# Kernel tuning notes

Measured on AMD Instinct MI355X. Metric: run time of the kernel, lower is better.

## Reference

```python
import jax, jax.numpy as jnp
import numpy as np

N_NODES = 100000
N_EDGES = 3200000
N_FEAT = 512
HIDDEN = 16
N_LABELS = 64


def gcn_layer(x, frm, to, W, b, n_nodes):
    # Original removes existing self-loops then adds one self-loop per node.
    # Equivalent jit-friendly form: zero-mask self-loop edges, add +1 to every
    # node's degree and an explicit self-loop term deg^-0.5 * deg^-0.5 * xw.
    mask = (frm != to).astype(x.dtype)                      # [E]
    deg = jax.ops.segment_sum(mask, to, num_segments=n_nodes) + 1.0  # [N], >=1 so no inf
    dis = deg ** -0.5                                        # [N]
    ew = dis[frm] * mask * dis[to]                           # [E]
    xw = x @ W                                               # [N, out]
    msgs = xw[frm] * ew[:, None]                             # gather-multiply  [E, out]
    agg = jax.ops.segment_sum(msgs, to, num_segments=n_nodes)  # scatter-add [N, out]
    out = agg + xw * (dis * dis)[:, None] + b                # self-loop weight = dis[i]^2
    return out


def setup_inputs() -> dict:
    key = jax.random.key(0)
    k1, k2, k3, k4 = jax.random.split(key, 4)
    x = jax.random.normal(k1, (N_NODES, N_FEAT), dtype=jnp.float32)
    edge_index = jax.random.randint(k2, (2, N_EDGES), 0, N_NODES, dtype=jnp.int32)
    # Xavier-uniform linear weights, zero bias (reset_paramters)
    lim1 = float(np.sqrt(6.0 / (N_FEAT + HIDDEN)))
    W1 = jax.random.uniform(k3, (N_FEAT, HIDDEN), jnp.float32, -lim1, lim1)
    b1 = jnp.zeros((HIDDEN,), jnp.float32)
    lim2 = float(np.sqrt(6.0 / (HIDDEN + N_LABELS)))
    W2 = jax.random.uniform(k4, (HIDDEN, N_LABELS), jnp.float32, -lim2, lim2)
    b2 = jnp.zeros((N_LABELS,), jnp.float32)
    return {"x": x, "edge_index": edge_index, "W1": W1, "b1": b1, "W2": W2, "b2": b2}


def reference(x, edge_index, W1, b1, W2, b2):
    n = x.shape[0]
    frm, to = edge_index[0], edge_index[1]
    h = jax.nn.relu(gcn_layer(x, frm, to, W1, b1, n))
    # dropout is identity in eval mode
    logits = gcn_layer(h, frm, to, W2, b2, n)
    return jax.nn.log_softmax(logits, axis=1)
```

## Files before the change

kernel.cpp:

```cpp
#include <hip/hip_runtime.h>
#include <hip/hip_fp16.h>
#include <cstdint>
#include <cstddef>

#define N_NODES 100000
#define N_FEAT  512
#define HIDDEN  16
#define N_LABELS 64
#define N_EDGES 3200000

#define NB    782
#define NPAD  (NB * 128)
#define CAP   4608
#define EPB   4096
#define BIN_BLOCKS 782
#define SPLITK 4

static const size_t O_GCUR = 0;
static const size_t O_DIS  = (size_t)16 << 10;
static const size_t O_STA  = (size_t)420 << 10;
static const size_t O_END  = (size_t)824 << 10;
static const size_t O_XWS  = (size_t)1228 << 10;
static const size_t O_HS   = (size_t)4360 << 10;
static const size_t O_TMP  = (size_t)7492 << 10;
static const size_t O_PART = (size_t)21572 << 10;
#define PART_STRIDE_H ((size_t)NPAD * 16)

__global__ __launch_bounds__(512) void k_bin(const int* __restrict__ frm,
                                             const int* __restrict__ to,
                                             int* __restrict__ gcur,
                                             unsigned* __restrict__ tmp) {
    __shared__ unsigned short barr[EPB];
    __shared__ int hist[NB + 1];
    __shared__ int gbase[NB];
    __shared__ int lcur[NB];
    const int t = threadIdx.x;
    const size_t e0 = (size_t)blockIdx.x * EPB;

    for (int i = t; i < NB + 1; i += 512) hist[i] = 0;
    __syncthreads();

    #pragma unroll
    for (int i = t; i < EPB; i += 512) {
        size_t e = e0 + i;
        int b = NB;
        if (e < N_EDGES) {
            int f = frm[e], tt = to[e];
            if (f != tt) b = tt >> 7;
        }
        barr[i] = (unsigned short)b;
        atomicAdd(&hist[b], 1);
    }
    __syncthreads();

    for (int b = t; b < NB; b += 512) {
        gbase[b] = atomicAdd(&gcur[b], hist[b]);
        lcur[b] = 0;
    }
    __syncthreads();

    #pragma unroll
    for (int i = t; i < EPB; i += 512) {
        int b = barr[i];
        if (b < NB) {
            size_t e = e0 + i;
            int f = frm[e], tt = to[e];
            int r = atomicAdd(&lcur[b], 1);
            int p = gbase[b] + r;
            if (p < CAP)
                tmp[(size_t)b * CAP + p] = ((unsigned)f << 7) | (unsigned)(tt & 127);
        }
    }
}

__global__ __launch_bounds__(512) void k_sort(unsigned* __restrict__ tmp,
                                              const int* __restrict__ gcur,
                                              int* __restrict__ starts,
                                              int* __restrict__ ends,
                                              float* __restrict__ dis) {
    __shared__ unsigned stage[CAP];
    __shared__ int cnt[128];
    __shared__ int sc[128];
    __shared__ int lcur[128];
    const int t = threadIdx.x, b = blockIdx.x;
    const int n_e = min(gcur[b], CAP);
    unsigned* seg = tmp + (size_t)b * CAP;

    if (t < 128) { cnt[t] = 0; lcur[t] = 0; }
    __syncthreads();

    for (int i = t; i < n_e; i += 512) {
        unsigned w = seg[i];
        stage[i] = w;
        atomicAdd(&cnt[w & 127u], 1);
    }
    __syncthreads();

    if (t < 128) sc[t] = cnt[t];
    __syncthreads();
    #pragma unroll
    for (int off = 1; off < 128; off <<= 1) {
        int a = 0;
        if (t < 128 && t >= off) a = sc[t - off];
        __syncthreads();
        if (t < 128) sc[t] += a;
        __syncthreads();
    }

    if (t < 128) {
        int excl = sc[t] - cnt[t];
        int node = b * 128 + t;
        int s0 = b * CAP + excl;
        starts[node] = s0;
        ends[node]   = s0 + cnt[t];
        dis[node]    = rsqrtf((float)cnt[t] + 1.0f);
    }
    __syncthreads();

    for (int i = t; i < n_e; i += 512) {
        unsigned w = stage[i];
        int tl = (int)(w & 127u);
        int p = atomicAdd(&lcur[tl], 1);
        seg[(sc[tl] - cnt[tl]) + p] = w >> 7;
    }
}

#define KT 32
__global__ __launch_bounds__(256) void k_gemm1(const float* __restrict__ x,
                                               const float* __restrict__ W1,
                                               __half* __restrict__ part) {
    __shared__ float xs[256 * 33];
    const int t = threadIdx.x;
    const int base = blockIdx.x * 256;
    const int kb = blockIdx.y * (N_FEAT / SPLITK);
    float acc[HIDDEN];
    #pragma unroll
    for (int j = 0; j < HIDDEN; ++j) acc[j] = 0.f;

    const int pr = t >> 3;
    const int pc = (t & 7) * 4;

    for (int kt = 0; kt < N_FEAT / SPLITK / KT; ++kt) {
        __syncthreads();
        #pragma unroll
        for (int p = 0; p < 8; ++p) {
            int r = p * 32 + pr;
            int n = base + r;
            float4 v = make_float4(0.f, 0.f, 0.f, 0.f);
            if (n < N_NODES)
                v = *(const float4*)(x + (size_t)n * N_FEAT + kb + kt * KT + pc);
            xs[r * 33 + pc + 0] = v.x;
            xs[r * 33 + pc + 1] = v.y;
            xs[r * 33 + pc + 2] = v.z;
            xs[r * 33 + pc + 3] = v.w;
        }
        __syncthreads();
        #pragma unroll
        for (int kk = 0; kk < KT; ++kk) {
            float xv = xs[t * 33 + kk];
            const float4* wr = (const float4*)(W1 + ((size_t)(kb + kt * KT + kk) << 4));
            float4 wa = wr[0], wb = wr[1], wc = wr[2], wd = wr[3];
            acc[ 0] = fmaf(xv, wa.x, acc[ 0]);
            acc[ 1] = fmaf(xv, wa.y, acc[ 1]);
            acc[ 2] = fmaf(xv, wa.z, acc[ 2]);
            acc[ 3] = fmaf(xv, wa.w, acc[ 3]);
            acc[ 4] = fmaf(xv, wb.x, acc[ 4]);
            acc[ 5] = fmaf(xv, wb.y, acc[ 5]);
            acc[ 6] = fmaf(xv, wb.z, acc[ 6]);
            acc[ 7] = fmaf(xv, wb.w, acc[ 7]);
            acc[ 8] = fmaf(xv, wc.x, acc[ 8]);
            acc[ 9] = fmaf(xv, wc.y, acc[ 9]);
            acc[10] = fmaf(xv, wc.z, acc[10]);
            acc[11] = fmaf(xv, wc.w, acc[11]);
            acc[12] = fmaf(xv, wd.x, acc[12]);
            acc[13] = fmaf(xv, wd.y, acc[13]);
            acc[14] = fmaf(xv, wd.z, acc[14]);
            acc[15] = fmaf(xv, wd.w, acc[15]);
        }
    }
    int n = base + t;
    if (n < N_NODES) {
        __half2 h2[8];
        #pragma unroll
        for (int j = 0; j < 8; ++j)
            h2[j] = __float22half2_rn(make_float2(acc[2 * j], acc[2 * j + 1]));
        float4* o = (float4*)(part + (size_t)blockIdx.y * PART_STRIDE_H + (size_t)n * HIDDEN);
        o[0] = *(float4*)&h2[0];
        o[1] = *(float4*)&h2[4];
    }
}

__global__ __launch_bounds__(256) void k_comb(const __half2* __restrict__ part2,
                                              const float* __restrict__ dis,
                                              __half2* __restrict__ xws2) {
    int i = blockIdx.x * 256 + threadIdx.x;
    if (i >= N_NODES * 8) return;
    const size_t st = (size_t)NPAD * 8;
    float2 a = __half22float2(part2[i]);
    float2 b = __half22float2(part2[st + i]);
    float2 c = __half22float2(part2[2 * st + i]);
    float2 d = __half22float2(part2[3 * st + i]);
    float dn = dis[i >> 3];
    xws2[i] = __float22half2_rn(make_float2(dn * (a.x + b.x + c.x + d.x),
                                            dn * (a.y + b.y + c.y + d.y)));
}

__global__ __launch_bounds__(512) void k_agg(const __half* __restrict__ rows,
                                             const unsigned* __restrict__ sorted,
                                             const int* __restrict__ starts,
                                             const int* __restrict__ ends,
                                             const float* __restrict__ dis,
                                             const float* __restrict__ bias,
                                             __half* __restrict__ outp,
                                             int mode) {
    const int t = threadIdx.x;
    const int lane = t & 15, g = t >> 4;
    const int n = blockIdx.x * 32 + g;
    const int s0 = starts[n], e0 = ends[n];
    float acc = 0.f;
    for (int base = s0; base < e0; base += 16) {
        int idx = base + lane;
        unsigned f = (idx < e0) ? sorted[idx] : 0u;
        int cnt = min(16, e0 - base);
        #pragma unroll
        for (int q = 0; q < 16; ++q) {
            unsigned fq = __shfl(f, q, 16);
            float v = __half2float(rows[(size_t)fq * HIDDEN + lane]);
            if (q < cnt) acc += v;
        }
    }
    if (n < N_NODES) {
        float dn = dis[n];
        float sum = acc + __half2float(rows[(size_t)n * HIDDEN + lane]);
        float v;
        if (mode) v = fmaxf(fmaf(dn, sum, bias[lane]), 0.f) * dn;
        else      v = dn * sum;
        outp[(size_t)n * HIDDEN + lane] = __float2half(v);
    }
}

__global__ __launch_bounds__(256) void k_out(const __half* __restrict__ z,
                                             const float* __restrict__ W2,
                                             const float* __restrict__ b2,
                                             float* __restrict__ out) {
    int gt = blockIdx.x * 256 + threadIdx.x;
    int n = gt >> 6;
    int j = gt & 63;
    float acc = b2[j];
    const __half* zr = z + (size_t)n * HIDDEN;
    #pragma unroll
    for (int k = 0; k < HIDDEN; ++k)
        acc = fmaf(__half2float(zr[k]), W2[k * N_LABELS + j], acc);
    float m = acc;
    #pragma unroll
    for (int off = 32; off > 0; off >>= 1)
        m = fmaxf(m, __shfl_xor(m, off, 64));
    float ex = __expf(acc - m);
    float sum = ex;
    #pragma unroll
    for (int off = 32; off > 0; off >>= 1)
        sum += __shfl_xor(sum, off, 64);
    out[(size_t)n * N_LABELS + j] = acc - m - __logf(sum);
}

extern "C" void kernel_launch(void* const* d_in, const int* in_sizes, int n_in,
                              void* d_out, int out_size, void* d_ws, size_t ws_size,
                              hipStream_t stream) {
    const float* x  = (const float*)d_in[0];
    const int*   ei = (const int*)d_in[1];
    const float* W1 = (const float*)d_in[2];
    const float* b1 = (const float*)d_in[3];
    const float* W2 = (const float*)d_in[4];
    const float* b2 = (const float*)d_in[5];
    float* out = (float*)d_out;
    char*  ws  = (char*)d_ws;

    int*      gcur   = (int*)(ws + O_GCUR);
    float*    dis    = (float*)(ws + O_DIS);
    int*      starts = (int*)(ws + O_STA);
    int*      ends   = (int*)(ws + O_END);
    __half*   xws    = (__half*)(ws + O_XWS);
    __half*   hs     = (__half*)(ws + O_HS);
    unsigned* tmp    = (unsigned*)(ws + O_TMP);
    __half*   part   = (__half*)(ws + O_PART);

    const int* frm = ei;
    const int* to  = ei + N_EDGES;

    hipMemsetAsync(gcur, 0, NB * sizeof(int), stream);

    k_bin  <<<BIN_BLOCKS, 512, 0, stream>>>(frm, to, gcur, tmp);
    k_sort <<<NB, 512, 0, stream>>>(tmp, gcur, starts, ends, dis);
    k_gemm1<<<dim3(391, SPLITK), 256, 0, stream>>>(x, W1, part);
    k_comb <<<3125, 256, 0, stream>>>((const __half2*)part, dis, (__half2*)xws);
    k_agg  <<<NPAD / 32, 512, 0, stream>>>(xws, tmp, starts, ends, dis, b1, hs, 1);
    k_agg  <<<NPAD / 32, 512, 0, stream>>>(hs, tmp, starts, ends, dis, b1, xws, 0);
    k_out  <<<N_NODES / 4, 256, 0, stream>>>(xws, W2, b2, out);
}
```

Baseline: 472.4 us.

## Fuse edge binning and split-K first GEMM into one heterogeneous launch

Merges the edge-binning kernel and the x@W1 split-K GEMM into a single launch. Block indices below BIN_BLOCKS do binning and the rest do GEMM tiles, so the memory-bound binning and the x streaming can overlap and one launch is saved. Binning now caches the packed edge word in shared memory so the scatter pass does not reload frm/to. The GEMM tile becomes 512 rows with a K-tile of 16 in a shared-memory union, which raises per-block shared usage and register pressure for the binning blocks and may lower occupancy.

```diff
diff --git a/kernel.cpp b/kernel.cpp
--- a/kernel.cpp
+++ b/kernel.cpp
@@ -15,6 +15,7 @@
 #define EPB   4096
 #define BIN_BLOCKS 782
 #define SPLITK 4
+#define GBLK  196
 
 static const size_t O_GCUR = 0;
 static const size_t O_DIS  = (size_t)16 << 10;
@@ -26,49 +27,131 @@
 static const size_t O_PART = (size_t)21572 << 10;
 #define PART_STRIDE_H ((size_t)NPAD * 16)
 
-__global__ __launch_bounds__(512) void k_bin(const int* __restrict__ frm,
-                                             const int* __restrict__ to,
-                                             int* __restrict__ gcur,
-                                             unsigned* __restrict__ tmp) {
-    __shared__ unsigned short barr[EPB];
-    __shared__ int hist[NB + 1];
-    __shared__ int gbase[NB];
-    __shared__ int lcur[NB];
+struct BinSh {
+    unsigned short barr[EPB];
+    unsigned       pk[EPB];
+    int hist[NB + 1];
+    int gbase[NB];
+    int lcur[NB];
+};
+union SMemBG {
+    BinSh bin;
+    float xs[512 * 17];
+};
+
+__global__ __launch_bounds__(512) void k_bg(const int* __restrict__ frm,
+                                            const int* __restrict__ to,
+                                            int* __restrict__ gcur,
+                                            unsigned* __restrict__ tmp,
+                                            const float* __restrict__ x,
+                                            const float* __restrict__ W1,
+                                            __half* __restrict__ part) {
+    __shared__ SMemBG sm;
     const int t = threadIdx.x;
-    const size_t e0 = (size_t)blockIdx.x * EPB;
-
-    for (int i = t; i < NB + 1; i += 512) hist[i] = 0;
-    __syncthreads();
-
-    #pragma unroll
-    for (int i = t; i < EPB; i += 512) {
-        size_t e = e0 + i;
-        int b = NB;
-        if (e < N_EDGES) {
-            int f = frm[e], tt = to[e];
-            if (f != tt) b = tt >> 7;
-        }
-        barr[i] = (unsigned short)b;
-        atomicAdd(&hist[b], 1);
-    }
-    __syncthreads();
-
-    for (int b = t; b < NB; b += 512) {
-        gbase[b] = atomicAdd(&gcur[b], hist[b]);
-        lcur[b] = 0;
-    }
-    __syncthreads();
-
-    #pragma unroll
-    for (int i = t; i < EPB; i += 512) {
-        int b = barr[i];
-        if (b < NB) {
+    const int bid = blockIdx.x;
+
+    if (bid < BIN_BLOCKS) {
+        BinSh& B = sm.bin;
+        const size_t e0 = (size_t)bid * EPB;
+
+        for (int i = t; i < NB + 1; i += 512) B.hist[i] = 0;
+        __syncthreads();
+
+        #pragma unroll
+        for (int i = t; i < EPB; i += 512) {
             size_t e = e0 + i;
-            int f = frm[e], tt = to[e];
-            int r = atomicAdd(&lcur[b], 1);
-            int p = gbase[b] + r;
-            if (p < CAP)
-                tmp[(size_t)b * CAP + p] = ((unsigned)f << 7) | (unsigned)(tt & 127);
+            int b = NB;
+            unsigned pk = 0;
+            if (e < N_EDGES) {
+                int f = frm[e], tt = to[e];
+                if (f != tt) {
+                    b = tt >> 7;
+                    pk = ((unsigned)f << 7) | (unsigned)(tt & 127);
+                }
+            }
+            B.barr[i] = (unsigned short)b;
+            B.pk[i] = pk;
+            atomicAdd(&B.hist[b], 1);
+        }
+        __syncthreads();
+
+        for (int b = t; b < NB; b += 512) {
+            B.gbase[b] = atomicAdd(&gcur[b], B.hist[b]);
+            B.lcur[b] = 0;
+        }
+        __syncthreads();
+
+        #pragma unroll
+        for (int i = t; i < EPB; i += 512) {
+            int b = B.barr[i];
+            if (b < NB) {
+                int r = atomicAdd(&B.lcur[b], 1);
+                int p = B.gbase[b] + r;
+                if (p < CAP)
+                    tmp[(size_t)b * CAP + p] = B.pk[i];
+            }
+        }
+    } else {
+        const int g = bid - BIN_BLOCKS;
+        const int split = g / GBLK;
+        const int bx = g - split * GBLK;
+        const int base = bx * 512;
+        const int kb = split * 128;
+
+        float acc[HIDDEN];
+        #pragma unroll
+        for (int j = 0; j < HIDDEN; ++j) acc[j] = 0.f;
+
+        const int pr = t >> 2;
+        const int pc = (t & 3) << 2;
+
+        for (int kt = 0; kt < 8; ++kt) {
+            __syncthreads();
+            #pragma unroll
+            for (int p = 0; p < 4; ++p) {
+                int r = p * 128 + pr;
+                int n = base + r;
+                float4 v = make_float4(0.f, 0.f, 0.f, 0.f);
+                if (n < N_NODES)
+                    v = *(const float4*)(x + (size_t)n * N_FEAT + kb + kt * 16 + pc);
+                sm.xs[r * 17 + pc + 0] = v.x;
+                sm.xs[r * 17 + pc + 1] = v.y;
+                sm.xs[r * 17 + pc + 2] = v.z;
+                sm.xs[r * 17 + pc + 3] = v.w;
+            }
+            __syncthreads();
+            #pragma unroll
+            for (int kk = 0; kk < 16; ++kk) {
+                float xv = sm.xs[t * 17 + kk];
+                const float4* wr = (const float4*)(W1 + ((size_t)(kb + kt * 16 + kk) << 4));
+                float4 wa = wr[0], wb = wr[1], wc = wr[2], wd = wr[3];
+                acc[ 0] = fmaf(xv, wa.x, acc[ 0]);
+                acc[ 1] = fmaf(xv, wa.y, acc[ 1]);
+                acc[ 2] = fmaf(xv, wa.z, acc[ 2]);
+                acc[ 3] = fmaf(xv, wa.w, acc[ 3]);
+                acc[ 4] = fmaf(xv, wb.x, acc[ 4]);
+                acc[ 5] = fmaf(xv, wb.y, acc[ 5]);
+                acc[ 6] = fmaf(xv, wb.z, acc[ 6]);
+                acc[ 7] = fmaf(xv, wb.w, acc[ 7]);
+                acc[ 8] = fmaf(xv, wc.x, acc[ 8]);
+                acc[ 9] = fmaf(xv, wc.y, acc[ 9]);
+                acc[10] = fmaf(xv, wc.z, acc[10]);
+                acc[11] = fmaf(xv, wc.w, acc[11]);
+                acc[12] = fmaf(xv, wd.x, acc[12]);
+                acc[13] = fmaf(xv, wd.y, acc[13]);
+                acc[14] = fmaf(xv, wd.z, acc[14]);
+                acc[15] = fmaf(xv, wd.w, acc[15]);
+            }
+        }
+        int n = base + t;
+        if (n < N_NODES) {
+            __half2 h2[8];
+            #pragma unroll
+            for (int j = 0; j < 8; ++j)
+                h2[j] = __float22half2_rn(make_float2(acc[2 * j], acc[2 * j + 1]));
+            float4* o = (float4*)(part + (size_t)split * PART_STRIDE_H + (size_t)n * HIDDEN);
+            o[0] = *(float4*)&h2[0];
+            o[1] = *(float4*)&h2[4];
         }
     }
 }
@@ -122,71 +205,6 @@
         int tl = (int)(w & 127u);
         int p = atomicAdd(&lcur[tl], 1);
         seg[(sc[tl] - cnt[tl]) + p] = w >> 7;
-    }
-}
-
-#define KT 32
-__global__ __launch_bounds__(256) void k_gemm1(const float* __restrict__ x,
-                                               const float* __restrict__ W1,
-                                               __half* __restrict__ part) {
-    __shared__ float xs[256 * 33];
-    const int t = threadIdx.x;
-    const int base = blockIdx.x * 256;
-    const int kb = blockIdx.y * (N_FEAT / SPLITK);
-    float acc[HIDDEN];
-    #pragma unroll
-    for (int j = 0; j < HIDDEN; ++j) acc[j] = 0.f;
-
-    const int pr = t >> 3;
-    const int pc = (t & 7) * 4;
-
-    for (int kt = 0; kt < N_FEAT / SPLITK / KT; ++kt) {
-        __syncthreads();
-        #pragma unroll
-        for (int p = 0; p < 8; ++p) {
-            int r = p * 32 + pr;
-            int n = base + r;
-            float4 v = make_float4(0.f, 0.f, 0.f, 0.f);
-            if (n < N_NODES)
-                v = *(const float4*)(x + (size_t)n * N_FEAT + kb + kt * KT + pc);
-            xs[r * 33 + pc + 0] = v.x;
-            xs[r * 33 + pc + 1] = v.y;
-            xs[r * 33 + pc + 2] = v.z;
-            xs[r * 33 + pc + 3] = v.w;
-        }
-        __syncthreads();
-        #pragma unroll
-        for (int kk = 0; kk < KT; ++kk) {
-            float xv = xs[t * 33 + kk];
-            const float4* wr = (const float4*)(W1 + ((size_t)(kb + kt * KT + kk) << 4));
-            float4 wa = wr[0], wb = wr[1], wc = wr[2], wd = wr[3];
-            acc[ 0] = fmaf(xv, wa.x, acc[ 0]);
-            acc[ 1] = fmaf(xv, wa.y, acc[ 1]);
-            acc[ 2] = fmaf(xv, wa.z, acc[ 2]);
-            acc[ 3] = fmaf(xv, wa.w, acc[ 3]);
-            acc[ 4] = fmaf(xv, wb.x, acc[ 4]);
-            acc[ 5] = fmaf(xv, wb.y, acc[ 5]);
-            acc[ 6] = fmaf(xv, wb.z, acc[ 6]);
-            acc[ 7] = fmaf(xv, wb.w, acc[ 7]);
-            acc[ 8] = fmaf(xv, wc.x, acc[ 8]);
-            acc[ 9] = fmaf(xv, wc.y, acc[ 9]);
-            acc[10] = fmaf(xv, wc.z, acc[10]);
-            acc[11] = fmaf(xv, wc.w, acc[11]);
-            acc[12] = fmaf(xv, wd.x, acc[12]);
-            acc[13] = fmaf(xv, wd.y, acc[13]);
-            acc[14] = fmaf(xv, wd.z, acc[14]);
-            acc[15] = fmaf(xv, wd.w, acc[15]);
-        }
-    }
-    int n = base + t;
-    if (n < N_NODES) {
-        __half2 h2[8];
-        #pragma unroll
-        for (int j = 0; j < 8; ++j)
-            h2[j] = __float22half2_rn(make_float2(acc[2 * j], acc[2 * j + 1]));
-        float4* o = (float4*)(part + (size_t)blockIdx.y * PART_STRIDE_H + (size_t)n * HIDDEN);
-        o[0] = *(float4*)&h2[0];
-        o[1] = *(float4*)&h2[4];
     }
 }
 
@@ -289,9 +307,8 @@
 
     hipMemsetAsync(gcur, 0, NB * sizeof(int), stream);
 
-    k_bin  <<<BIN_BLOCKS, 512, 0, stream>>>(frm, to, gcur, tmp);
+    k_bg   <<<BIN_BLOCKS + SPLITK * GBLK, 512, 0, stream>>>(frm, to, gcur, tmp, x, W1, part);
     k_sort <<<NB, 512, 0, stream>>>(tmp, gcur, starts, ends, dis);
-    k_gemm1<<<dim3(391, SPLITK), 256, 0, stream>>>(x, W1, part);
     k_comb <<<3125, 256, 0, stream>>>((const __half2*)part, dis, (__half2*)xws);
     k_agg  <<<NPAD / 32, 512, 0, stream>>>(xws, tmp, starts, ends, dis, b1, hs, 1);
     k_agg  <<<NPAD / 32, 512, 0, stream>>>(hs, tmp, starts, ends, dis, b1, xws, 0);
```

After: 457.4 us. 3.2% less time.
